# Kernel tuning notes

Measured on AMD Instinct MI355X. Metric: run time of the kernel, lower is better.

Reference implementation:

```python
import jax, jax.numpy as jnp
import numpy as np
from jax.ops import segment_sum

GRID = 32        # cells per axis; offset grid is (GRID+1)^3
T = 48           # number of accepted MC topologies
N_PTS = 131072

# 12 cube edges: base (lower) corner offset and axis the edge runs along.
# e0..3: x/y edges of z=0 face, e4..7: same at z=1, e8..11: vertical z edges.
EDGE_BASE = np.array([[0,0,0],[1,0,0],[0,1,0],[0,0,0],
                      [0,0,1],[1,0,1],[0,1,1],[0,0,1],
                      [0,0,0],[1,0,0],[1,1,0],[0,1,0]], dtype=np.int32)
EDGE_AXIS = np.array([0,1,0,1, 0,1,0,1, 2,2,2,2], dtype=np.int32)
EDGE_DIR  = np.eye(3, dtype=np.float32)[EDGE_AXIS]          # [12,3] unit dirs


def _dot(u, v):
    return jnp.sum(u * v, axis=-1)


def _safe_div(n, d, eps=1e-12):
    return n / jnp.where(jnp.abs(d) > eps, d, eps)


def _point_tri_dist_sq(p, a, b, c):
    """Squared distance from p to triangle (a,b,c); Ericson closest-point
    algorithm with full vertex/edge/interior region clamping, vectorized.
    p broadcasts against a/b/c over leading dims; last dim is xyz."""
    ab = b - a; ac = c - a; ap = p - a
    d1 = _dot(ab, ap); d2 = _dot(ac, ap)
    bp = p - b; d3 = _dot(ab, bp); d4 = _dot(ac, bp)
    cp = p - c; d5 = _dot(ab, cp); d6 = _dot(ac, cp)
    vc = d1 * d4 - d3 * d2
    vb = d5 * d2 - d1 * d6
    va = d3 * d6 - d5 * d4
    v_ab = _safe_div(d1, d1 - d3)
    w_ac = _safe_div(d2, d2 - d6)
    w_bc = _safe_div(d4 - d3, (d4 - d3) + (d5 - d6))
    inv = _safe_div(jnp.ones_like(va), va + vb + vc)
    v_in = vb * inv; w_in = vc * inv
    q = a + ab * v_in[..., None] + ac * w_in[..., None]                      # interior
    q = jnp.where(((va <= 0) & ((d4 - d3) >= 0) & ((d5 - d6) >= 0))[..., None],
                  b + (c - b) * w_bc[..., None], q)                          # edge BC
    q = jnp.where(((vb <= 0) & (d2 >= 0) & (d6 <= 0))[..., None],
                  a + ac * w_ac[..., None], q)                               # edge AC
    q = jnp.where(((d6 >= 0) & (d5 <= d6))[..., None], c, q)                 # vertex C
    q = jnp.where(((vc <= 0) & (d1 >= 0) & (d3 <= 0))[..., None],
                  a + ab * v_ab[..., None], q)                               # edge AB
    q = jnp.where(((d3 >= 0) & (d4 <= d3))[..., None], b, q)                 # vertex B
    q = jnp.where(((d1 <= 0) & (d2 <= 0))[..., None], a, q)                  # vertex A
    diff = p - q
    return _dot(diff, diff)


def setup_inputs() -> dict:
    key = jax.random.key(0)
    k1, k2, k3 = jax.random.split(key, 3)
    offset = jax.random.uniform(k1, (3, GRID + 1, GRID + 1, GRID + 1), dtype=jnp.float32)
    points = jax.random.uniform(k2, (N_PTS, 3), dtype=jnp.float32) * GRID
    tri_table = jax.random.randint(k3, (T, 3, 3), 0, 12, dtype=jnp.int32)
    return {"offset": offset, "points": points, "tri_table": tri_table}


def reference(offset, points, tri_table):
    edge_base_i = jnp.asarray(EDGE_BASE)                 # [12,3] int
    edge_base_f = jnp.asarray(EDGE_BASE, dtype=offset.dtype)
    edge_dir = jnp.asarray(EDGE_DIR, dtype=offset.dtype)
    edge_axis = jnp.asarray(EDGE_AXIS)

    cell = jnp.clip(jnp.floor(points).astype(jnp.int32), 0, GRID - 1)   # [N,3]
    local = points - cell.astype(points.dtype)                          # [N,3] in [0,1)^3

    # grid index of each edge's base corner -> edge offset parameter t in [0,1]
    gidx = cell[:, None, :] + edge_base_i[None, :, :]                   # [N,12,3]
    t = offset[edge_axis[None, :], gidx[..., 0], gidx[..., 1], gidx[..., 2]]  # [N,12]
    verts = edge_base_f[None] + edge_dir[None] * t[..., None]           # [N,12,3] local coords

    tri = verts[:, tri_table]                                           # [N,T,3tri,3vert,3]
    a = tri[:, :, :, 0, :]; b = tri[:, :, :, 1, :]; c = tri[:, :, :, 2, :]
    p = local[:, None, None, :]                                         # [N,1,1,3]
    d2 = _point_tri_dist_sq(p, a, b, c)                                 # [N,T,3]
    d_min = jnp.min(d2, axis=-1)                                        # [N,T]

    cell_id = (cell[:, 0] * GRID + cell[:, 1]) * GRID + cell[:, 2]      # [N]
    distances_full = segment_sum(d_min, cell_id, num_segments=GRID ** 3)  # [GRID^3, T]
    return distances_full
```

## Files before the change

kernel.cpp:

```cpp
#include <hip/hip_runtime.h>

#define GRID 32
#define NT 48
#define BLK 256
#define SPLIT 16
#define PPB (BLK / SPLIT)

#define EDGE_PACK ( (0ULL<<0) | (9ULL<<5) | (2ULL<<10) | (8ULL<<15) | \
                    (4ULL<<20) | (13ULL<<25) | (6ULL<<30) | (12ULL<<35) | \
                    (16ULL<<40) | (17ULL<<45) | (19ULL<<50) | (18ULL<<55) )

__device__ __forceinline__ float tri_dist_gram(float AA, float AB, float AC,
                                               float BB, float BC, float CC) {
    float d1 = AA - AB, d2 = AA - AC;
    float d3 = AB - BB, d4 = AB - BC;
    float d5 = AC - BC, d6 = AC - CC;
    float d43 = BB - BC;
    float d56 = CC - BC;
    float vc = d1 * d4 - d3 * d2;
    float vb = d5 * d2 - d1 * d6;
    float va = d3 * d6 - d5 * d4;

    bool cbc = (va <= 0.f) & (d43 >= 0.f) & (d56 >= 0.f);
    bool cac = (vb <= 0.f) & (d2 >= 0.f) & (d6 <= 0.f);
    bool ccc = (d6 >= 0.f) & (d5 <= d6);
    bool cab = (vc <= 0.f) & (d1 >= 0.f) & (d3 <= 0.f);
    bool cbb = (d3 >= 0.f) & (d4 <= d3);
    bool caa = (d1 <= 0.f) & (d2 <= 0.f);

    float nv = vb, nw = vc, den = va + vb + vc;
    bool mode = false;
    nw = cbc ? d43 : nw;  den = cbc ? d43 + d56 : den;  mode = cbc ? true  : mode;
    nv = cac ? 0.f : nv;  nw = cac ? d2  : nw;  den = cac ? d2 - d6 : den;  mode = cac ? false : mode;
    nw = ccc ? 1.f : nw;  den = ccc ? 1.f : den;  mode = ccc ? true  : mode;
    nv = cab ? d1  : nv;  nw = cab ? 0.f : nw;  den = cab ? d1 - d3 : den;  mode = cab ? false : mode;
    nw = cbb ? 0.f : nw;  den = cbb ? 1.f : den;  mode = cbb ? true  : mode;
    nv = caa ? 0.f : nv;  nw = caa ? 0.f : nw;  den = caa ? 1.f : den;  mode = caa ? false : mode;

    float dd  = (fabsf(den) > 1e-12f) ? den : 1e-12f;
    float inv = __builtin_amdgcn_rcpf(dd);
    float vp = nv * inv;
    float wp = nw * inv;
    float u = mode ? 0.f : 1.f - vp - wp;
    float v = mode ? 1.f - wp : vp;
    float e1 = fmaf(AC, wp, fmaf(AB, v, AA * u));
    float e2 = fmaf(BC, wp, fmaf(BB, v, AB * u));
    float e3 = fmaf(CC, wp, fmaf(BC, v, AC * u));
    return fmaf(wp, e3, fmaf(v, e2, u * e1));
}

__global__ __launch_bounds__(BLK) void ptd_kernel(
    const float* __restrict__ offset,
    const float* __restrict__ points,
    const int*   __restrict__ tri_table,
    float*       __restrict__ out,
    int n)
{
    __shared__ float4 v_s[PPB * 13];
    __shared__ float  gram[PPB * 144];
    __shared__ int2   goff[NT * 3];

    const int tid = threadIdx.x;
    const int g   = blockIdx.x * BLK + tid;
    const int pt  = g >> 4;
    const int grp = tid & 15;
    const int pl  = tid >> 4;
    const bool active = (pt < n);

    if (tid < NT * 3) {
        int i = tri_table[tid * 3 + 0];
        int j = tri_table[tid * 3 + 1];
        int k = tri_table[tid * 3 + 2];
        int o0 = (i * 13) | ((i * 12 + j) << 8) | ((i * 12 + k) << 16);
        int o1 = (j * 13) | ((j * 12 + k) << 8) | ((k * 13) << 16);
        goff[tid] = make_int2(o0, o1);
    }

    float4 vi = make_float4(0.f, 0.f, 0.f, 0.f);
    int cx = 0, cy = 0, cz = 0;
    if (active) {
        float px = points[pt * 3 + 0];
        float py = points[pt * 3 + 1];
        float pz = points[pt * 3 + 2];
        cx = min(max((int)floorf(px), 0), GRID - 1);
        cy = min(max((int)floorf(py), 0), GRID - 1);
        cz = min(max((int)floorf(pz), 0), GRID - 1);
        if (grp < 12) {
            float lx = px - (float)cx;
            float ly = py - (float)cy;
            float lz = pz - (float)cz;
            unsigned nib = (unsigned)(EDGE_PACK >> (5 * grp)) & 31u;
            int gx = cx + (int)(nib & 1u);
            int gy = cy + (int)((nib >> 1) & 1u);
            int gz = cz + (int)((nib >> 2) & 1u);
            int ax = (int)(nib >> 3);
            float t = offset[((ax * 33 + gx) * 33 + gy) * 33 + gz];
            float vx = (ax == 0) ? t : (float)(nib & 1u);
            float vy = (ax == 1) ? t : (float)((nib >> 1) & 1u);
            float vz = (ax == 2) ? t : (float)((nib >> 2) & 1u);
            vi = make_float4(lx - vx, ly - vy, lz - vz, 0.0f);
            v_s[pl * 13 + grp] = vi;
        }
    }
    __syncthreads();

    if (active && grp < 12) {
        float* gp = &gram[pl * 144];
        int j = grp;
#pragma unroll
        for (int d = 0; d < 7; d++) {
            float4 vj = v_s[pl * 13 + j];
            float dv = fmaf(vi.z, vj.z, fmaf(vi.y, vj.y, vi.x * vj.x));
            gp[grp * 12 + j] = dv;
            gp[j * 12 + grp] = dv;
            j = (j == 11) ? 0 : j + 1;
        }
    }
    __syncthreads();

    if (!active) return;

    const float* gp = &gram[pl * 144];
    float* outp = out + ((((cx * GRID) + cy) * GRID + cz) * NT);
    const int2* gofft = &goff[grp * 9];

#pragma unroll
    for (int r = 0; r < 3; r++) {
        float dmin;
#pragma unroll
        for (int k = 0; k < 3; k++) {
            int2 o = gofft[r * 3 + k];
            float AA = gp[o.x & 255];
            float AB = gp[(o.x >> 8) & 255];
            float AC = gp[(unsigned)o.x >> 16];
            float BB = gp[o.y & 255];
            float BC = gp[(o.y >> 8) & 255];
            float CC = gp[(unsigned)o.y >> 16];
            float d = tri_dist_gram(AA, AB, AC, BB, BC, CC);
            dmin = (k == 0) ? d : fminf(dmin, d);
        }
        atomicAdd(&outp[grp * 3 + r], dmin);
    }
}

extern "C" void kernel_launch(void* const* d_in, const int* in_sizes, int n_in,
                              void* d_out, int out_size, void* d_ws, size_t ws_size,
                              hipStream_t stream) {
    const float* offset    = (const float*)d_in[0];
    const float* points    = (const float*)d_in[1];
    const int*   tri_table = (const int*)d_in[2];
    float* out = (float*)d_out;
    int n = in_sizes[1] / 3;

    hipMemsetAsync(d_out, 0, (size_t)out_size * sizeof(float), stream);

    long total = (long)n * SPLIT;
    int blocks = (int)((total + BLK - 1) / BLK);
    ptd_kernel<<<blocks, BLK, 0, stream>>>(offset, points, tri_table, out, n);
}
```

Baseline: 127.1 us.

## Bin points by cell and accumulate per-cell sums in shared memory

Adds a binning pass that places each point into a per-cell work list, with an overflow list for cells holding more than 32 points. A cell-major kernel then processes 16 cells per block, accumulates the per-topology sums in shared memory and writes the output once, replacing global atomics and the output memset. Every block also scans the whole overflow list, there is an extra launch, and occupancy is uneven across cells. The new path is only taken when the workspace is large enough; otherwise the original kernel runs.

```diff
diff --git a/kernel.cpp b/kernel.cpp
--- a/kernel.cpp
+++ b/kernel.cpp
@@ -5,6 +5,8 @@
 #define BLK 256
 #define SPLIT 16
 #define PPB (BLK / SPLIT)
+#define NCELLS (GRID * GRID * GRID)
+#define CAP 32
 
 #define EDGE_PACK ( (0ULL<<0) | (9ULL<<5) | (2ULL<<10) | (8ULL<<15) | \
                     (4ULL<<20) | (13ULL<<25) | (6ULL<<30) | (12ULL<<35) | \
@@ -47,6 +49,181 @@
     float e2 = fmaf(BC, wp, fmaf(BB, v, AB * u));
     float e3 = fmaf(CC, wp, fmaf(BC, v, AC * u));
     return fmaf(wp, e3, fmaf(v, e2, u * e1));
+}
+
+__device__ __forceinline__ void process_round(
+    bool act, int pt, int cellid, int cl,
+    const float* __restrict__ offset,
+    const float* __restrict__ points,
+    float4* v_s, float* gram, const int2* goff, float* acc,
+    int pl, int grp)
+{
+    float4 vi = make_float4(0.f, 0.f, 0.f, 0.f);
+    if (act && grp < 12) {
+        float px = points[pt * 3 + 0];
+        float py = points[pt * 3 + 1];
+        float pz = points[pt * 3 + 2];
+        int cx = cellid >> 10, cy = (cellid >> 5) & 31, cz = cellid & 31;
+        float lx = px - (float)cx;
+        float ly = py - (float)cy;
+        float lz = pz - (float)cz;
+        unsigned nib = (unsigned)(EDGE_PACK >> (5 * grp)) & 31u;
+        int gx = cx + (int)(nib & 1u);
+        int gy = cy + (int)((nib >> 1) & 1u);
+        int gz = cz + (int)((nib >> 2) & 1u);
+        int ax = (int)(nib >> 3);
+        float t = offset[((ax * 33 + gx) * 33 + gy) * 33 + gz];
+        float vx = (ax == 0) ? t : (float)(nib & 1u);
+        float vy = (ax == 1) ? t : (float)((nib >> 1) & 1u);
+        float vz = (ax == 2) ? t : (float)((nib >> 2) & 1u);
+        vi = make_float4(lx - vx, ly - vy, lz - vz, 0.0f);
+        v_s[pl * 13 + grp] = vi;
+    }
+    __syncthreads();
+    if (act && grp < 12) {
+        float* gp = &gram[pl * 144];
+        int j = grp;
+#pragma unroll
+        for (int d = 0; d < 7; d++) {
+            float4 vj = v_s[pl * 13 + j];
+            float dv = fmaf(vi.z, vj.z, fmaf(vi.y, vj.y, vi.x * vj.x));
+            gp[grp * 12 + j] = dv;
+            gp[j * 12 + grp] = dv;
+            j = (j == 11) ? 0 : j + 1;
+        }
+    }
+    __syncthreads();
+    if (act) {
+        const float* gp = &gram[pl * 144];
+        const int2* gofft = &goff[grp * 9];
+        float* accp = &acc[cl * NT + grp * 3];
+#pragma unroll
+        for (int r = 0; r < 3; r++) {
+            float dmin;
+#pragma unroll
+            for (int k = 0; k < 3; k++) {
+                int2 o = gofft[r * 3 + k];
+                float AA = gp[o.x & 255];
+                float AB = gp[(o.x >> 8) & 255];
+                float AC = gp[(unsigned)o.x >> 16];
+                float BB = gp[o.y & 255];
+                float BC = gp[(o.y >> 8) & 255];
+                float CC = gp[(unsigned)o.y >> 16];
+                float d = tri_dist_gram(AA, AB, AC, BB, BC, CC);
+                dmin = (k == 0) ? d : fminf(dmin, d);
+            }
+            atomicAdd(&accp[r], dmin);
+        }
+    }
+}
+
+__global__ __launch_bounds__(256) void bin_kernel(
+    const float* __restrict__ points, int n,
+    int* __restrict__ cnt, int* __restrict__ wlist,
+    int* __restrict__ ovf_cnt, int* __restrict__ ovf)
+{
+    int pt = blockIdx.x * 256 + threadIdx.x;
+    if (pt >= n) return;
+    float px = points[pt * 3 + 0];
+    float py = points[pt * 3 + 1];
+    float pz = points[pt * 3 + 2];
+    int cx = min(max((int)floorf(px), 0), GRID - 1);
+    int cy = min(max((int)floorf(py), 0), GRID - 1);
+    int cz = min(max((int)floorf(pz), 0), GRID - 1);
+    int cellid = ((cx * GRID) + cy) * GRID + cz;
+    int pos = atomicAdd(&cnt[cellid], 1);
+    if (pos < CAP) wlist[cellid * CAP + pos] = pt;
+    else { int e = atomicAdd(ovf_cnt, 1); ovf[e] = pt; }
+}
+
+__global__ __launch_bounds__(BLK) void cell_kernel(
+    const float* __restrict__ offset,
+    const float* __restrict__ points,
+    const int*   __restrict__ tri_table,
+    const int*   __restrict__ cnt,
+    const int*   __restrict__ wlist,
+    const int*   __restrict__ ovf_cnt,
+    const int*   __restrict__ ovf,
+    float*       __restrict__ out)
+{
+    __shared__ float4 v_s[PPB * 13];
+    __shared__ float  gram[PPB * 144];
+    __shared__ int2   goff[NT * 3];
+    __shared__ float  acc[PPB * NT];
+    __shared__ unsigned short qmap[PPB * CAP];
+    __shared__ int    offs_s[PPB + 1];
+    __shared__ int    cnt_s[PPB];
+    __shared__ int    movf_s;
+
+    const int tid = threadIdx.x;
+    const int grp = tid & 15;
+    const int pl  = tid >> 4;
+    const int c0  = blockIdx.x * PPB;
+
+    if (tid < NT * 3) {
+        int i = tri_table[tid * 3 + 0];
+        int j = tri_table[tid * 3 + 1];
+        int k = tri_table[tid * 3 + 2];
+        int o0 = (i * 13) | ((i * 12 + j) << 8) | ((i * 12 + k) << 16);
+        int o1 = (j * 13) | ((j * 12 + k) << 8) | ((k * 13) << 16);
+        goff[tid] = make_int2(o0, o1);
+    }
+    if (tid < PPB) cnt_s[tid] = min(cnt[c0 + tid], CAP);
+    if (tid == 0) movf_s = *ovf_cnt;
+    acc[tid] = 0.f; acc[tid + 256] = 0.f; acc[tid + 512] = 0.f;
+    __syncthreads();
+    if (tid == 0) {
+        int s = 0;
+#pragma unroll
+        for (int i = 0; i < PPB; i++) { offs_s[i] = s; s += cnt_s[i]; }
+        offs_s[PPB] = s;
+    }
+    __syncthreads();
+    if (tid < PPB) {
+        int o = offs_s[tid], c = cnt_s[tid];
+        for (int i = 0; i < c; i++) qmap[o + i] = (unsigned short)((tid << 5) | i);
+    }
+    const int T_b = offs_s[PPB];
+    const int movf = movf_s;
+    __syncthreads();
+
+    const int nr = (T_b + PPB - 1) >> 4;
+    for (int m = 0; m < nr; m++) {
+        int q = m * PPB + pl;
+        bool act = (q < T_b);
+        int pt = 0, cellid = 0, cl = 0;
+        if (act) {
+            int v = qmap[q];
+            cl = v >> 5;
+            int i = v & 31;
+            pt = wlist[(c0 + cl) * CAP + i];
+            cellid = c0 + cl;
+        }
+        process_round(act, pt, cellid, cl, offset, points, v_s, gram, goff, acc, pl, grp);
+    }
+
+    for (int base = 0; base < movf; base += PPB) {
+        int j = base + pl;
+        bool act = false; int pt = 0, cellid = 0, cl = 0;
+        if (j < movf) {
+            pt = ovf[j];
+            float px = points[pt * 3 + 0];
+            float py = points[pt * 3 + 1];
+            float pz = points[pt * 3 + 2];
+            int cx = min(max((int)floorf(px), 0), GRID - 1);
+            int cy = min(max((int)floorf(py), 0), GRID - 1);
+            int cz = min(max((int)floorf(pz), 0), GRID - 1);
+            cellid = ((cx * GRID) + cy) * GRID + cz;
+            cl = cellid - c0;
+            act = (cl >= 0) && (cl < PPB);
+        }
+        process_round(act, pt, cellid, cl, offset, points, v_s, gram, goff, acc, pl, grp);
+    }
+
+    __syncthreads();
+    out[c0 * NT + tid]       = acc[tid];
+    out[c0 * NT + tid + 256] = acc[tid + 256];
+    out[c0 * NT + tid + 512] = acc[tid + 512];
 }
 
 __global__ __launch_bounds__(BLK) void ptd_kernel(
@@ -103,7 +280,6 @@
         }
     }
     __syncthreads();
-
     if (active && grp < 12) {
         float* gp = &gram[pl * 144];
         int j = grp;
@@ -117,13 +293,11 @@
         }
     }
     __syncthreads();
-
     if (!active) return;
 
     const float* gp = &gram[pl * 144];
     float* outp = out + ((((cx * GRID) + cy) * GRID + cz) * NT);
     const int2* gofft = &goff[grp * 9];
-
 #pragma unroll
     for (int r = 0; r < 3; r++) {
         float dmin;
@@ -152,9 +326,27 @@
     float* out = (float*)d_out;
     int n = in_sizes[1] / 3;
 
-    hipMemsetAsync(d_out, 0, (size_t)out_size * sizeof(float), stream);
-
-    long total = (long)n * SPLIT;
-    int blocks = (int)((total + BLK - 1) / BLK);
-    ptd_kernel<<<blocks, BLK, 0, stream>>>(offset, points, tri_table, out, n);
-}
+    const size_t CNT_BYTES = (size_t)NCELLS * 4;
+    const size_t OVFC_OFF  = CNT_BYTES;
+    const size_t WL_OFF    = CNT_BYTES + 128;
+    const size_t WL_BYTES  = (size_t)NCELLS * CAP * 4;
+    const size_t OVF_OFF   = WL_OFF + WL_BYTES;
+    const size_t WS_NEED   = OVF_OFF + (size_t)n * 4;
+
+    if (ws_size >= WS_NEED) {
+        char* ws = (char*)d_ws;
+        int* cnt     = (int*)(ws);
+        int* ovf_cnt = (int*)(ws + OVFC_OFF);
+        int* wlist   = (int*)(ws + WL_OFF);
+        int* ovf     = (int*)(ws + OVF_OFF);
+        hipMemsetAsync(ws, 0, WL_OFF, stream);
+        bin_kernel<<<(n + 255) / 256, 256, 0, stream>>>(points, n, cnt, wlist, ovf_cnt, ovf);
+        cell_kernel<<<NCELLS / PPB, BLK, 0, stream>>>(offset, points, tri_table,
+                                                      cnt, wlist, ovf_cnt, ovf, out);
+    } else {
+        hipMemsetAsync(d_out, 0, (size_t)out_size * sizeof(float), stream);
+        long total = (long)n * SPLIT;
+        int blocks = (int)((total + BLK - 1) / BLK);
+        ptd_kernel<<<blocks, BLK, 0, stream>>>(offset, points, tri_table, out, n);
+    }
+}
```

Measured after the change: 145.3 us. 14.3% more time.
